# Kernel tuning notes

Measured on AMD Instinct MI355X. Metric: run time of the kernel, lower is better.

The kernel has to match this reference:

```python
import jax, jax.numpy as jnp
import numpy as np

D = 512; N = 1536; H = 4; DH = D // H
MAX_INT = 5; BINS = 100; LAYERS = 3


def _mha(q_in, k_in, v_in, in_w, in_b, out_w, out_b):
    """PyTorch-style nn.MultiheadAttention (batch of 1). Returns (out [Nq,D], head-avg weights [Nq,Nk])."""
    wq, wk, wv = in_w[:D], in_w[D:2 * D], in_w[2 * D:]
    bq, bk, bv = in_b[:D], in_b[D:2 * D], in_b[2 * D:]
    n_q, n_k = q_in.shape[0], k_in.shape[0]
    q = (q_in @ wq.T + bq).reshape(n_q, H, DH).transpose(1, 0, 2)  # [H,Nq,dh]
    k = (k_in @ wk.T + bk).reshape(n_k, H, DH).transpose(1, 0, 2)
    v = (v_in @ wv.T + bv).reshape(n_k, H, DH).transpose(1, 0, 2)
    scores = jnp.einsum('hqd,hkd->hqk', q, k) / jnp.sqrt(jnp.asarray(DH, q.dtype))
    w = jax.nn.softmax(scores, axis=-1)  # [H,Nq,Nk]
    out = jnp.einsum('hqk,hkd->hqd', w, v).transpose(1, 0, 2).reshape(n_q, D)
    out = out @ out_w.T + out_b
    return out, w.mean(0)


def setup_inputs() -> dict:
    key = jax.random.key(0)
    ks = jax.random.split(key, 12)
    s = 0.02
    return {
        'node_embeddings': jax.random.normal(ks[0], (N, D), jnp.float32),
        'time_positions': jax.random.uniform(ks[1], (N, 1), jnp.float32) * 10.0,
        'batch_indices': jnp.zeros((N,), jnp.int32),
        'W_time': jax.random.normal(ks[2], (D, 1), jnp.float32) * s,
        'b_time': jnp.zeros((D,), jnp.float32),
        'in_w': jax.random.normal(ks[3], (3 * D, D), jnp.float32) * s,
        'in_b': jnp.zeros((3 * D,), jnp.float32),
        'out_w': jax.random.normal(ks[4], (D, D), jnp.float32) * s,
        'out_b': jnp.zeros((D,), jnp.float32),
        'ic_w1': jax.random.normal(ks[5], (128, D), jnp.float32) * s,
        'ic_b1': jnp.zeros((128,), jnp.float32),
        'ic_w2': jax.random.normal(ks[6], (MAX_INT, 128), jnp.float32) * s,
        'ic_b2': jnp.zeros((MAX_INT,), jnp.float32),
        'ref_w1': jax.random.normal(ks[7], (LAYERS, 128, D + 2), jnp.float32) * s,
        'ref_b1': jnp.zeros((LAYERS, 128), jnp.float32),
        'ref_w2': jax.random.normal(ks[8], (LAYERS, 2 * BINS, 128), jnp.float32) * s,
        'ref_b2': jnp.zeros((LAYERS, 2 * BINS), jnp.float32),
        'weight_params': jnp.linspace(-0.5, 0.5, BINS).astype(jnp.float32),
        'qp_w': jax.random.normal(ks[9], (D, D + 2), jnp.float32) * s,
        'qp_b': jnp.zeros((D,), jnp.float32),
    }


def _forward(node_embeddings, time_positions, W_time, b_time, in_w, in_b, out_w, out_b,
             ic_w1, ic_b1, ic_w2, ic_b2, ref_w1, ref_b1, ref_w2, ref_b2,
             weight_params, qp_w, qp_b):
    x = node_embeddings + time_positions @ W_time.T + b_time  # [N,D]
    attn_out, _ = _mha(x, x, x, in_w, in_b, out_w, out_b)      # [N,D]
    pooled = attn_out.mean(0)                                   # [D]
    probs = jax.nn.softmax(ic_w2 @ jax.nn.relu(ic_w1 @ pooled + ic_b1) + ic_b2)
    num_intervals = jnp.argmax(probs) + 1
    interval_mask = jnp.arange(MAX_INT) < num_intervals
    t_min, t_max = time_positions.min(), time_positions.max()
    grid = jnp.linspace(t_min, t_max, MAX_INT + 1)
    start, end = grid[:-1], grid[1:]                            # [MAX_INT]
    n = attn_out.shape[0]
    ones = jnp.ones((n, 1), attn_out.dtype)

    def per_interval(s_i, e_i, w1, b1, w2, b2):
        query = jnp.concatenate([attn_out, ones * s_i, ones * e_i], axis=-1)  # [N,D+2]
        qp = query @ qp_w.T + qp_b                                            # [N,D]
        h = jax.nn.relu(query @ w1.T + b1)
        logits = h @ w2.T + b2                                                # [N,2*BINS]
        s_off = (jax.nn.softmax(logits[:, :BINS], axis=-1) * weight_params).sum(-1)  # [N]
        e_off = (jax.nn.softmax(logits[:, BINS:], axis=-1) * weight_params).sum(-1)
        _, aw = _mha(qp, attn_out, attn_out, in_w, in_b, out_w, out_b)        # [N,N]
        return (aw * s_off).sum(), (aw * e_off).sum()

    for l in range(LAYERS):  # layers have distinct params; intervals are independent within a layer
        ds, de = jax.vmap(per_interval, in_axes=(0, 0, None, None, None, None))(
            start, end, ref_w1[l], ref_b1[l], ref_w2[l], ref_b2[l])
        start = start + ds
        end = end + de

    final_bounds = jnp.stack([start, end], axis=-1)  # [MAX_INT,2]
    return final_bounds, interval_mask


def reference(node_embeddings, time_positions, batch_indices, W_time, b_time, in_w, in_b,
              out_w, out_b, ic_w1, ic_b1, ic_w2, ic_b2, ref_w1, ref_b1, ref_w2, ref_b2,
              weight_params, qp_w, qp_b):
    return _forward(node_embeddings, time_positions, W_time, b_time, in_w, in_b, out_w, out_b,
                    ic_w1, ic_b1, ic_w2, ic_b2, ref_w1, ref_b1, ref_w2, ref_b2,
                    weight_params, qp_w, qp_b)
```

## Files before the change

### kernel.cpp

```cpp
#include <hip/hip_runtime.h>
#include <hip/hip_bf16.h>

typedef __hip_bfloat16 bf16;
typedef __bf16 bf16x8 __attribute__((ext_vector_type(8)));
typedef float f32x4 __attribute__((ext_vector_type(4)));

#define DD   512
#define NT   1536
#define NH   4
#define DHD  128
#define NBINS 100
#define MAXI 5
#define NL   3
#define RSQRT_DH 0.08838834764831845f

#define OFF_X      ((size_t)0)
#define OFF_QKV    (OFF_X    + (size_t)NT*DD)
#define OFF_ATT    (OFF_QKV  + (size_t)NT*3*DD)
#define OFF_CTX    (OFF_ATT  + (size_t)NT*DD)
#define OFF_K2     (OFF_CTX  + (size_t)NT*DD)
#define OFF_QP0    (OFF_K2   + (size_t)NT*DD)
#define OFF_Q0     (OFF_QP0  + (size_t)NT*DD)
#define OFF_H0     (OFF_Q0   + (size_t)NT*DD)
#define OFF_HR     (OFF_H0   + (size_t)NT*384)
#define OFF_LG     (OFF_HR   + (size_t)MAXI*NT*128)
#define OFF_AARR   (OFF_LG   + (size_t)MAXI*NT*200)
#define OFF_BARR   (OFF_AARR + (size_t)NH*NT)
#define OFF_AV     (OFF_BARR + (size_t)NH*NT)
#define OFF_BV     (OFF_AV   + (size_t)DD)
#define OFF_SOFF   (OFF_BV   + (size_t)DD)
#define OFF_EOFF   (OFF_SOFF + (size_t)MAXI*NT)
#define OFF_RST    (OFF_EOFF + (size_t)MAXI*NT)
#define OFF_POOL   (OFF_RST  + (size_t)NH*NT*2)
#define OFF_SCAL   (OFF_POOL + (size_t)DD)
#define OFF_S      (OFF_SCAL + (size_t)64)
#define SC_START 0
#define SC_END   5
#define SC_DSDE  10
#define SC_CNT   20
#define OFF_M2   (OFF_QP0 + (size_t)512*512)
#define OFF_B2   (OFF_QP0 + (size_t)2*512*512)
#define PSLICE   ((size_t)NH*NT*16)
#define OFF_STAT (OFF_LG + (size_t)8*PSLICE)

__global__ __launch_bounds__(256) void k_misc(
    const float* __restrict__ tpos, const float* __restrict__ in_w,
    const float* __restrict__ in_b, const float* __restrict__ qp_w,
    const float* __restrict__ qp_b, float* ws)
{
    __shared__ __bf16 As[64 * 40];
    __shared__ __bf16 Bs[64 * 40];
    __shared__ float smn[256], smx[256];
    int bx = blockIdx.x, tid = threadIdx.x;
    if (bx < 64) {
        int m0 = (bx >> 3) * 64, n0 = (bx & 7) * 64;
        int r = tid >> 2, quad = tid & 3;
        int w = tid >> 6, lane = tid & 63;
        int wm = (w & 1) * 32, wn = (w >> 1) * 32;
        int lr = lane & 15, lq = lane >> 4;
        f32x4 acc[2][2];
#pragma unroll
        for (int i = 0; i < 2; i++)
#pragma unroll
            for (int j = 0; j < 2; j++) acc[i][j] = (f32x4){0.f, 0.f, 0.f, 0.f};
        const float* arow = in_w + (size_t)(m0 + r) * DD + quad * 8;
        int kk = tid >> 3, g = tid & 7;
        for (int k0 = 0; k0 < DD; k0 += 32) {
            __bf16 ta[8] __attribute__((aligned(16)));
#pragma unroll
            for (int q = 0; q < 4; q++) {
                float2 f = *(const float2*)(arow + k0 + 2 * q);
                ta[2 * q] = (__bf16)f.x; ta[2 * q + 1] = (__bf16)f.y;
            }
            const float* bsrc = qp_w + (size_t)(k0 + kk) * 514 + n0 + g * 8;
            float4 b0 = *(const float4*)bsrc;
            float4 b1 = *(const float4*)(bsrc + 4);
            float bb[8] = {b0.x, b0.y, b0.z, b0.w, b1.x, b1.y, b1.z, b1.w};
            __syncthreads();
            *(bf16x8*)&As[r * 40 + quad * 8] = *(bf16x8*)ta;
#pragma unroll
            for (int q = 0; q < 8; q++) Bs[(g * 8 + q) * 40 + kk] = (__bf16)bb[q];
            __syncthreads();
            bf16x8 af[2], bfr[2];
#pragma unroll
            for (int i = 0; i < 2; i++) af[i] = *(bf16x8*)&As[(wm + i * 16 + lr) * 40 + lq * 8];
#pragma unroll
            for (int j = 0; j < 2; j++) bfr[j] = *(bf16x8*)&Bs[(wn + j * 16 + lr) * 40 + lq * 8];
#pragma unroll
            for (int i = 0; i < 2; i++)
#pragma unroll
                for (int j = 0; j < 2; j++)
                    acc[i][j] = __builtin_amdgcn_mfma_f32_16x16x32_bf16(af[i], bfr[j], acc[i][j], 0, 0, 0);
        }
        float* M2 = ws + OFF_M2;
#pragma unroll
        for (int i = 0; i < 2; i++)
#pragma unroll
            for (int r4 = 0; r4 < 4; r4++) {
                int gm = m0 + wm + i * 16 + lq * 4 + r4;
#pragma unroll
                for (int j = 0; j < 2; j++)
                    M2[(size_t)gm * 512 + n0 + wn + j * 16 + lr] = acc[i][j][r4];
            }
    } else if (bx < 72) {
        int w = tid >> 6, lane = tid & 63;
        float su8[8], sv8[8], sb8[8];
#pragma unroll
        for (int q = 0; q < 8; q++) {
            int c = lane * 8 + q;
            su8[q] = qp_w[(size_t)c * 514 + 512];
            sv8[q] = qp_w[(size_t)c * 514 + 513];
            sb8[q] = qp_b[c];
        }
        int base = (bx - 64) * 64 + w * 16;
        for (int t = 0; t < 16; t++) {
            int row = base + t;
            const float* wr = in_w + (size_t)row * DD + lane * 8;
            float4 x0 = *(const float4*)wr, x1 = *(const float4*)(wr + 4);
            float xa[8] = {x0.x, x0.y, x0.z, x0.w, x1.x, x1.y, x1.z, x1.w};
            float a = 0.f, b = 0.f, c2 = 0.f;
#pragma unroll
            for (int q = 0; q < 8; q++) { a += xa[q] * su8[q]; b += xa[q] * sv8[q]; c2 += xa[q] * sb8[q]; }
            for (int off = 32; off; off >>= 1) {
                a += __shfl_xor(a, off); b += __shfl_xor(b, off); c2 += __shfl_xor(c2, off);
            }
            if (lane == 0) {
                ws[OFF_AV + row] = a; ws[OFF_BV + row] = b; ws[OFF_B2 + row] = c2 + in_b[row];
            }
        }
    } else {
        ws[OFF_POOL + tid] = 0.f; ws[OFF_POOL + 256 + tid] = 0.f;
        float mn = 1e30f, mx = -1e30f;
        for (int i = tid; i < NT; i += 256) { float v = tpos[i]; mn = fminf(mn, v); mx = fmaxf(mx, v); }
        smn[tid] = mn; smx[tid] = mx; __syncthreads();
        for (int s = 128; s; s >>= 1) {
            if (tid < s) { smn[tid] = fminf(smn[tid], smn[tid + s]); smx[tid] = fmaxf(smx[tid], smx[tid + s]); }
            __syncthreads();
        }
        if (tid == 0) {
            float tmin = smn[0], tmax = smx[0];
            for (int i = 0; i < MAXI; i++) {
                ws[OFF_SCAL + SC_START + i] = tmin + (tmax - tmin) * (float)i / 5.0f;
                ws[OFF_SCAL + SC_END + i]   = tmin + (tmax - tmin) * (float)(i + 1) / 5.0f;
            }
        }
    }
}

__global__ __launch_bounds__(256) void k_score(
    const float* __restrict__ A, int lda, long long aZ,
    const float* __restrict__ B, int ldb, long long bZ,
    bf16* __restrict__ C, float* __restrict__ stat)
{
    int z = blockIdx.z;
    A += (size_t)z * aZ; B += (size_t)z * bZ;
    int m0 = blockIdx.y * 128, n0 = blockIdx.x * 128;
    __shared__ __bf16 As[128 * 40];
    __shared__ __bf16 Bs[128 * 40];
    __shared__ float sMax[4][64];
    __shared__ float sSum[4][64];
    int tid = threadIdx.x;
    int r = tid >> 1, hh = tid & 1;
    int w = tid >> 6, lane = tid & 63;
    int wm = (w & 1) * 64, wn = (w >> 1) * 64;
    int lr = lane & 15, lq = lane >> 4;
    f32x4 acc[4][4];
#pragma unroll
    for (int i = 0; i < 4; i++)
#pragma unroll
        for (int j = 0; j < 4; j++) acc[i][j] = (f32x4){0.f, 0.f, 0.f, 0.f};

    const float* arow = A + (size_t)(m0 + r) * lda + hh * 16;
    const float* brow = B + (size_t)(n0 + r) * ldb + hh * 16;
    __bf16* awr = &As[r * 40 + hh * 16];
    __bf16* bwr = &Bs[r * 40 + hh * 16];

    for (int k0 = 0; k0 < DHD; k0 += 32) {
        __bf16 ta[16] __attribute__((aligned(16)));
        __bf16 tb[16] __attribute__((aligned(16)));
#pragma unroll
        for (int q = 0; q < 8; q++) {
            float2 f = *(const float2*)(arow + k0 + 2 * q);
            ta[2 * q] = (__bf16)f.x; ta[2 * q + 1] = (__bf16)f.y;
            float2 g = *(const float2*)(brow + k0 + 2 * q);
            tb[2 * q] = (__bf16)g.x; tb[2 * q + 1] = (__bf16)g.y;
        }
        __syncthreads();
        *(bf16x8*)awr = *(bf16x8*)ta;
        *(bf16x8*)(awr + 8) = *(bf16x8*)(ta + 8);
        *(bf16x8*)bwr = *(bf16x8*)tb;
        *(bf16x8*)(bwr + 8) = *(bf16x8*)(tb + 8);
        __syncthreads();
        bf16x8 af[4], bfr[4];
#pragma unroll
        for (int i = 0; i < 4; i++) af[i] = *(bf16x8*)&As[(wm + i * 16 + lr) * 40 + lq * 8];
#pragma unroll
        for (int j = 0; j < 4; j++) bfr[j] = *(bf16x8*)&Bs[(wn + j * 16 + lr) * 40 + lq * 8];
#pragma unroll
        for (int i = 0; i < 4; i++)
#pragma unroll
            for (int j = 0; j < 4; j++)
                acc[i][j] = __builtin_amdgcn_mfma_f32_16x16x32_bf16(af[i], bfr[j], acc[i][j], 0, 0, 0);
    }
#pragma unroll
    for (int i = 0; i < 4; i++)
#pragma unroll
        for (int r4 = 0; r4 < 4; r4++) {
            int gm = m0 + wm + i * 16 + lq * 4 + r4;
#pragma unroll
            for (int j = 0; j < 4; j++) {
                int gn = n0 + wn + j * 16 + lr;
                C[(size_t)z * NT * NT + (size_t)gm * NT + gn] =
                    __float2bfloat16(acc[i][j][r4] * RSQRT_DH);
            }
        }
#pragma unroll
    for (int i = 0; i < 4; i++)
#pragma unroll
        for (int r4 = 0; r4 < 4; r4++) {
            float m = -1e30f;
#pragma unroll
            for (int j = 0; j < 4; j++) m = fmaxf(m, acc[i][j][r4] * RSQRT_DH);
            for (int off = 1; off < 16; off <<= 1) m = fmaxf(m, __shfl_xor(m, off));
            if (lr == 0) sMax[w][i * 16 + lq * 4 + r4] = m;
        }
    __syncthreads();
#pragma unroll
    for (int i = 0; i < 4; i++)
#pragma unroll
        for (int r4 = 0; r4 < 4; r4++) {
            int lidx = i * 16 + lq * 4 + r4;
            float M = fmaxf(sMax[w][lidx], sMax[w ^ 2][lidx]);
            float s = 0.f;
#pragma unroll
            for (int j = 0; j < 4; j++) s += __expf(acc[i][j][r4] * RSQRT_DH - M);
            for (int off = 1; off < 16; off <<= 1) s += __shfl_xor(s, off);
            if (lr == 0) sSum[w][lidx] = s;
        }
    __syncthreads();
    if (tid < 128) {
        int lidx = tid & 63, wb = tid >> 6;
        float M = fmaxf(sMax[wb][lidx], sMax[wb + 2][lidx]);
        float den = sSum[wb][lidx] + sSum[wb + 2][lidx];
        size_t base = ((size_t)z * NT + m0 + tid) * 24 + (size_t)blockIdx.x * 2;
        stat[base] = M; stat[base + 1] = den;
    }
}

__global__ __launch_bounds__(256) void k_qkv(
    const float* __restrict__ emb, const float* __restrict__ t,
    const float* __restrict__ wt, const float* __restrict__ bt,
    const float* __restrict__ in_w, const float* __restrict__ in_b, float* ws)
{
    int m0 = blockIdx.y * 64, n0 = blockIdx.x * 64;
    __shared__ __bf16 As[64 * 40];
    __shared__ __bf16 Bs[64 * 40];
    int tid = threadIdx.x;
    int r = tid >> 2, quad = tid & 3;
    int w = tid >> 6, lane = tid & 63;
    int wm = (w & 1) * 32, wn = (w >> 1) * 32;
    int lr = lane & 15, lq = lane >> 4;
    f32x4 acc[2][2];
#pragma unroll
    for (int i = 0; i < 2; i++)
#pragma unroll
        for (int j = 0; j < 2; j++) acc[i][j] = (f32x4){0.f, 0.f, 0.f, 0.f};

    float trow = t[m0 + r];
    const float* arow = emb + (size_t)(m0 + r) * DD + quad * 8;
    const float* brow = in_w + (size_t)(n0 + r) * DD + quad * 8;
    __bf16* awr = &As[r * 40 + quad * 8];
    __bf16* bwr = &Bs[r * 40 + quad * 8];

    for (int k0 = 0; k0 < DD; k0 += 32) {
        __bf16 ta[8] __attribute__((aligned(16)));
        __bf16 tb[8] __attribute__((aligned(16)));
#pragma unroll
        for (int q = 0; q < 4; q++) {
            float2 e = *(const float2*)(arow + k0 + 2 * q);
            float2 wv = *(const float2*)(wt + k0 + quad * 8 + 2 * q);
            float2 bv = *(const float2*)(bt + k0 + quad * 8 + 2 * q);
            ta[2 * q]     = (__bf16)(e.x + trow * wv.x + bv.x);
            ta[2 * q + 1] = (__bf16)(e.y + trow * wv.y + bv.y);
            float2 f = *(const float2*)(brow + k0 + 2 * q);
            tb[2 * q] = (__bf16)f.x; tb[2 * q + 1] = (__bf16)f.y;
        }
        __syncthreads();
        *(bf16x8*)awr = *(bf16x8*)ta;
        *(bf16x8*)bwr = *(bf16x8*)tb;
        __syncthreads();
        bf16x8 af[2], bfr[2];
#pragma unroll
        for (int i = 0; i < 2; i++) af[i] = *(bf16x8*)&As[(wm + i * 16 + lr) * 40 + lq * 8];
#pragma unroll
        for (int j = 0; j < 2; j++) bfr[j] = *(bf16x8*)&Bs[(wn + j * 16 + lr) * 40 + lq * 8];
#pragma unroll
        for (int i = 0; i < 2; i++)
#pragma unroll
            for (int j = 0; j < 2; j++)
                acc[i][j] = __builtin_amdgcn_mfma_f32_16x16x32_bf16(af[i], bfr[j], acc[i][j], 0, 0, 0);
    }
    float* qkv = ws + OFF_QKV;
    float* Vt  = ws + OFF_X;
#pragma unroll
    for (int i = 0; i < 2; i++)
#pragma unroll
        for (int j = 0; j < 2; j++) {
            int gn = n0 + wn + j * 16 + lr;
            int gmb = m0 + wm + i * 16 + lq * 4;
            float b = in_b[gn];
            f32x4 vv = acc[i][j];
            vv[0] += b; vv[1] += b; vv[2] += b; vv[3] += b;
            if (gn < 2 * DD) {
#pragma unroll
                for (int r4 = 0; r4 < 4; r4++)
                    qkv[(size_t)(gmb + r4) * (3 * DD) + gn] = vv[r4];
            } else {
                *(float4*)&Vt[(size_t)(gn - 2 * DD) * NT + gmb] = *(float4*)&vv;
            }
        }
}

__global__ __launch_bounds__(256) void k_pv(const bf16* __restrict__ S, float* ws) {
    int h = blockIdx.z;
    int m0 = blockIdx.y * 64;
    int n0 = (blockIdx.x & 1) * 64;
    int ks = blockIdx.x >> 1;
    const int KCH = NT / 2;
    int kbeg = ks * KCH;
    __shared__ __bf16 As[64 * 40];
    __shared__ __bf16 Bs[64 * 40];
    __shared__ float sM[64], sI[64];
    int tid = threadIdx.x;
    if (tid < 64) {
        const float* st = ws + OFF_STAT + ((size_t)(h * NT + m0 + tid)) * 24;
        float M = -1e30f;
#pragma unroll
        for (int t2 = 0; t2 < 12; t2++) M = fmaxf(M, st[2 * t2]);
        float den = 0.f;
#pragma unroll
        for (int t2 = 0; t2 < 12; t2++) den += st[2 * t2 + 1] * __expf(st[2 * t2] - M);
        sM[tid] = M; sI[tid] = 1.f / den;
    }
    __syncthreads();
    int r = tid >> 2, quad = tid & 3;
    int w = tid >> 6, lane = tid & 63;
    int wm = (w & 1) * 32, wn = (w >> 1) * 32;
    int lr = lane & 15, lq = lane >> 4;
    const float* Vt = ws + OFF_X + (size_t)h * DHD * NT;
    const bf16* Sh = S + (size_t)h * NT * NT;
    float mrow = sM[r];
    const unsigned short* srow = (const unsigned short*)(Sh + (size_t)(m0 + r) * NT) + quad * 8;
    const float* brow = Vt + (size_t)(n0 + r) * NT + quad * 8;
    __bf16* awr = &As[r * 40 + quad * 8];
    __bf16* bwr = &Bs[r * 40 + quad * 8];
    f32x4 acc[2][2];
#pragma unroll
    for (int i = 0; i < 2; i++)
#pragma unroll
        for (int j = 0; j < 2; j++) acc[i][j] = (f32x4){0.f, 0.f, 0.f, 0.f};

    for (int k0 = kbeg; k0 < kbeg + KCH; k0 += 32) {
        union { uint4 u; unsigned short s[8]; } bb;
        bb.u = *(const uint4*)(srow + k0);
        __bf16 ta[8] __attribute__((aligned(16)));
        __bf16 tb[8] __attribute__((aligned(16)));
#pragma unroll
        for (int q = 0; q < 8; q++)
            ta[q] = (__bf16)__expf(__uint_as_float((unsigned)bb.s[q] << 16) - mrow);
#pragma unroll
        for (int q = 0; q < 4; q++) {
            float2 f = *(const float2*)(brow + k0 + 2 * q);
            tb[2 * q] = (__bf16)f.x; tb[2 * q + 1] = (__bf16)f.y;
        }
        __syncthreads();
        *(bf16x8*)awr = *(bf16x8*)ta;
        *(bf16x8*)bwr = *(bf16x8*)tb;
        __syncthreads();
        bf16x8 af[2], bfr[2];
#pragma unroll
        for (int i = 0; i < 2; i++) af[i] = *(bf16x8*)&As[(wm + i * 16 + lr) * 40 + lq * 8];
#pragma unroll
        for (int j = 0; j < 2; j++) bfr[j] = *(bf16x8*)&Bs[(wn + j * 16 + lr) * 40 + lq * 8];
#pragma unroll
        for (int i = 0; i < 2; i++)
#pragma unroll
            for (int j = 0; j < 2; j++)
                acc[i][j] = __builtin_amdgcn_mfma_f32_16x16x32_bf16(af[i], bfr[j], acc[i][j], 0, 0, 0);
    }
    float* dst = ws + (ks == 0 ? OFF_CTX : OFF_HR);
#pragma unroll
    for (int i = 0; i < 2; i++)
#pragma unroll
        for (int r4 = 0; r4 < 4; r4++) {
            int lrow = wm + i * 16 + lq * 4 + r4;
            float ri = sI[lrow];
#pragma unroll
            for (int j = 0; j < 2; j++) {
                int gn = n0 + wn + j * 16 + lr;
                dst[(size_t)(m0 + lrow) * DD + h * DHD + gn] = acc[i][j][r4] * ri;
            }
        }
}

__global__ __launch_bounds__(256) void k_oproj(
    const float* __restrict__ out_w, const float* __restrict__ out_b, float* ws)
{
    int m0 = blockIdx.y * 64, n0 = blockIdx.x * 64;
    __shared__ __bf16 As[64 * 40];
    __shared__ __bf16 Bs[64 * 40];
    __shared__ float ps[64];
    int tid = threadIdx.x;
    int r = tid >> 2, quad = tid & 3;
    int w = tid >> 6, lane = tid & 63;
    int wm = (w & 1) * 32, wn = (w >> 1) * 32;
    int lr = lane & 15, lq = lane >> 4;
    f32x4 acc[2][2];
#pragma unroll
    for (int i = 0; i < 2; i++)
#pragma unroll
        for (int j = 0; j < 2; j++) acc[i][j] = (f32x4){0.f, 0.f, 0.f, 0.f};
    if (tid < 64) ps[tid] = 0.f;

    const float* a0 = ws + OFF_CTX + (size_t)(m0 + r) * DD + quad * 8;
    const float* a1 = ws + OFF_HR  + (size_t)(m0 + r) * DD + quad * 8;
    const float* brow = out_w + (size_t)(n0 + r) * DD + quad * 8;
    __bf16* awr = &As[r * 40 + quad * 8];
    __bf16* bwr = &Bs[r * 40 + quad * 8];

    for (int k0 = 0; k0 < DD; k0 += 32) {
        __bf16 ta[8] __attribute__((aligned(16)));
        __bf16 tb[8] __attribute__((aligned(16)));
#pragma unroll
        for (int q = 0; q < 4; q++) {
            float2 x = *(const float2*)(a0 + k0 + 2 * q);
            float2 y = *(const float2*)(a1 + k0 + 2 * q);
            ta[2 * q]     = (__bf16)(x.x + y.x);
            ta[2 * q + 1] = (__bf16)(x.y + y.y);
            float2 f = *(const float2*)(brow + k0 + 2 * q);
            tb[2 * q] = (__bf16)f.x; tb[2 * q + 1] = (__bf16)f.y;
        }
        __syncthreads();
        *(bf16x8*)awr = *(bf16x8*)ta;
        *(bf16x8*)bwr = *(bf16x8*)tb;
        __syncthreads();
        bf16x8 af[2], bfr[2];
#pragma unroll
        for (int i = 0; i < 2; i++) af[i] = *(bf16x8*)&As[(wm + i * 16 + lr) * 40 + lq * 8];
#pragma unroll
        for (int j = 0; j < 2; j++) bfr[j] = *(bf16x8*)&Bs[(wn + j * 16 + lr) * 40 + lq * 8];
#pragma unroll
        for (int i = 0; i < 2; i++)
#pragma unroll
            for (int j = 0; j < 2; j++)
                acc[i][j] = __builtin_amdgcn_mfma_f32_16x16x32_bf16(af[i], bfr[j], acc[i][j], 0, 0, 0);
    }
    float* att = ws + OFF_ATT;
#pragma unroll
    for (int j = 0; j < 2; j++) {
        int gn = n0 + wn + j * 16 + lr;
        float b = out_b[gn];
        float colsum = 0.f;
#pragma unroll
        for (int i = 0; i < 2; i++)
#pragma unroll
            for (int r4 = 0; r4 < 4; r4++) {
                int gm = m0 + wm + i * 16 + lq * 4 + r4;
                float v = acc[i][j][r4] + b;
                att[(size_t)gm * DD + gn] = v;
                colsum += v;
            }
        atomicAdd(&ps[wn + j * 16 + lr], colsum);
    }
    __syncthreads();
    if (tid < 64) atomicAdd(&ws[OFF_POOL + n0 + tid], ps[tid]);
}

__global__ __launch_bounds__(256) void k_trip(
    const float* __restrict__ in_w, const float* __restrict__ in_b,
    const float* __restrict__ ref_w1, const float* __restrict__ ref_b1,
    const float* __restrict__ icw1, const float* __restrict__ icb1,
    const float* __restrict__ icw2, const float* __restrict__ icb2,
    float* ws, float* out)
{
    __shared__ __bf16 As[64 * 40];
    __shared__ __bf16 Bs[64 * 40];
    __shared__ float h1[128];
    __shared__ float lg[MAXI];
    int bx = blockIdx.x, tid = threadIdx.x;
    if (bx == 22) {
        if (blockIdx.y != 0) return;
        int w = tid >> 6, lane = tid & 63;
        const float* pp = ws + OFF_POOL + lane * 8;
        float4 p0 = *(const float4*)pp, p1 = *(const float4*)(pp + 4);
        float p8[8] = {p0.x, p0.y, p0.z, p0.w, p1.x, p1.y, p1.z, p1.w};
        for (int t = 0; t < 32; t++) {
            int row = w * 32 + t;
            const float* wr = icw1 + (size_t)row * DD + lane * 8;
            float4 a = *(const float4*)wr, b = *(const float4*)(wr + 4);
            float d = a.x * p8[0] + a.y * p8[1] + a.z * p8[2] + a.w * p8[3]
                    + b.x * p8[4] + b.y * p8[5] + b.z * p8[6] + b.w * p8[7];
            for (int off = 32; off; off >>= 1) d += __shfl_xor(d, off);
            if (lane == 0) h1[row] = fmaxf(d * (1.0f / NT) + icb1[row], 0.f);
        }
        __syncthreads();
        if (tid < MAXI) {
            float s = icb2[tid];
            for (int j = 0; j < 128; j++) s += icw2[tid * 128 + j] * h1[j];
            lg[tid] = s;
        }
        __syncthreads();
        if (tid == 0) {
            int best = 0; float bv = lg[0];
            for (int m = 1; m < MAXI; m++) if (lg[m] > bv) { bv = lg[m]; best = m; }
            int ni = best + 1;
            for (int i = 0; i < MAXI; i++) out[10 + i] = (i < ni) ? 1.f : 0.f;
        }
        return;
    }
    const float* B; const float* bias; float* C; int ldb, ldc, n0;
    if (bx < 8)       { B = in_w + (size_t)DD * DD; ldb = DD;  bias = in_b + DD;   C = ws + OFF_K2; ldc = DD;  n0 = bx * 64; }
    else if (bx < 16) { B = ws + OFF_M2;            ldb = 512; bias = ws + OFF_B2; C = ws + OFF_Q0; ldc = DD;  n0 = (bx - 8) * 64; }
    else              { B = ref_w1;                 ldb = 514; bias = ref_b1;      C = ws + OFF_H0; ldc = 384; n0 = (bx - 16) * 64; }
    const float* A = ws + OFF_ATT;
    int m0 = blockIdx.y * 64;
    int r = tid >> 2, quad = tid & 3;
    int w = tid >> 6, lane = tid & 63;
    int wm = (w & 1) * 32, wn = (w >> 1) * 32;
    int lr = lane & 15, lq = lane >> 4;
    f32x4 acc[2][2];
#pragma unroll
    for (int i = 0; i < 2; i++)
#pragma unroll
        for (int j = 0; j < 2; j++) acc[i][j] = (f32x4){0.f, 0.f, 0.f, 0.f};

    const float* arow = A + (size_t)(m0 + r) * DD + quad * 8;
    const float* brow = B + (size_t)(n0 + r) * ldb + quad * 8;
    __bf16* awr = &As[r * 40 + quad * 8];
    __bf16* bwr = &Bs[r * 40 + quad * 8];

    for (int k0 = 0; k0 < DD; k0 += 32) {
        __bf16 ta[8] __attribute__((aligned(16)));
        __bf16 tb[8] __attribute__((aligned(16)));
#pragma unroll
        for (int q = 0; q < 4; q++) {
            float2 f = *(const float2*)(arow + k0 + 2 * q);
            ta[2 * q] = (__bf16)f.x; ta[2 * q + 1] = (__bf16)f.y;
            float2 g = *(const float2*)(brow + k0 + 2 * q);
            tb[2 * q] = (__bf16)g.x; tb[2 * q + 1] = (__bf16)g.y;
        }
        __syncthreads();
        *(bf16x8*)awr = *(bf16x8*)ta;
        *(bf16x8*)bwr = *(bf16x8*)tb;
        __syncthreads();
        bf16x8 af[2], bfr[2];
#pragma unroll
        for (int i = 0; i < 2; i++) af[i] = *(bf16x8*)&As[(wm + i * 16 + lr) * 40 + lq * 8];
#pragma unroll
        for (int j = 0; j < 2; j++) bfr[j] = *(bf16x8*)&Bs[(wn + j * 16 + lr) * 40 + lq * 8];
#pragma unroll
        for (int i = 0; i < 2; i++)
#pragma unroll
            for (int j = 0; j < 2; j++)
                acc[i][j] = __builtin_amdgcn_mfma_f32_16x16x32_bf16(af[i], bfr[j], acc[i][j], 0, 0, 0);
    }
#pragma unroll
    for (int i = 0; i < 2; i++)
#pragma unroll
        for (int r4 = 0; r4 < 4; r4++) {
            int gm = m0 + wm + i * 16 + lq * 4 + r4;
#pragma unroll
            for (int j = 0; j < 2; j++) {
                int gn = n0 + wn + j * 16 + lr;
                C[(size_t)gm * ldc + gn] = acc[i][j][r4] + bias[gn];
            }
        }
}

__global__ __launch_bounds__(256) void k_abc(float* ws) {
    int wave = threadIdx.x >> 6, lane = threadIdx.x & 63;
    int row = blockIdx.x * 4 + wave;
    int h = row / NT, n = row % NT;
    const float* k2 = ws + OFF_K2 + (size_t)n * DD + h * DHD;
    const float* av = ws + OFF_AV + h * DHD;
    const float* bv = ws + OFF_BV + h * DHD;
    int d = lane * 2;
    float a = av[d] * k2[d] + av[d + 1] * k2[d + 1];
    float b = bv[d] * k2[d] + bv[d + 1] * k2[d + 1];
    float tm = (lane < 12) ? ws[OFF_STAT + (size_t)row * 24 + lane * 2] : -1e30f;
    for (int off = 32; off; off >>= 1) { a += __shfl_xor(a, off); b += __shfl_xor(b, off); }
    for (int off = 1; off < 16; off <<= 1) tm = fmaxf(tm, __shfl_xor(tm, off));
    if (lane == 0) {
        ws[OFF_AARR + row] = a * RSQRT_DH;
        ws[OFF_BARR + row] = b * RSQRT_DH;
        ws[OFF_RST + row] = tm;
    }
}

__global__ __launch_bounds__(256) void k_lgs(
    const float* __restrict__ rw1, const float* __restrict__ rw2,
    const float* __restrict__ rb2, const float* __restrict__ wp, int l, float* ws)
{
    __shared__ float dsh[128];
    __shared__ __bf16 As[64 * 136];
    __shared__ __bf16 Bs[64 * 136];
    __shared__ __bf16 Ls[64 * 208];
    int tid = threadIdx.x;
    int m0 = blockIdx.x * 64;
    int i_int = m0 / NT;
    int nbase = m0 % NT;
    if (blockIdx.x == 0 && tid < 11) ws[OFF_SCAL + SC_DSDE + tid] = 0.f;
    if (tid < 128) {
        float s_i = ws[OFF_SCAL + SC_START + i_int], e_i = ws[OFF_SCAL + SC_END + i_int];
        const float* wr = rw1 + (size_t)(l * 128 + tid) * 514;
        dsh[tid] = s_i * wr[512] + e_i * wr[513];
    }
    __syncthreads();
    int r = tid >> 2, quad = tid & 3;
    {
        const float* arow = ws + OFF_H0 + (size_t)(nbase + r) * 384 + l * 128 + quad * 32;
        __bf16 tmp[32] __attribute__((aligned(16)));
#pragma unroll
        for (int q = 0; q < 16; q++) {
            float2 f = *(const float2*)(arow + 2 * q);
            int jj = quad * 32 + 2 * q;
            tmp[2 * q]     = (__bf16)fmaxf(f.x + dsh[jj], 0.f);
            tmp[2 * q + 1] = (__bf16)fmaxf(f.y + dsh[jj + 1], 0.f);
        }
        __bf16* aw = &As[r * 136 + quad * 32];
#pragma unroll
        for (int q = 0; q < 4; q++) *(bf16x8*)(aw + q * 8) = *(bf16x8*)(tmp + q * 8);
    }
    int w = tid >> 6, lane = tid & 63;
    int wm = (w & 1) * 32, wn = (w >> 1) * 32;
    int lr = lane & 15, lq = lane >> 4;
    for (int nt = 0; nt < 4; nt++) {
        int n0 = nt * 64;
        int gnr = n0 + r;
        __bf16 tmp[32] __attribute__((aligned(16)));
        if (gnr < 200) {
            const float* brow = rw2 + (size_t)gnr * 128 + quad * 32;
#pragma unroll
            for (int q = 0; q < 16; q++) {
                float2 f = *(const float2*)(brow + 2 * q);
                tmp[2 * q] = (__bf16)f.x; tmp[2 * q + 1] = (__bf16)f.y;
            }
        } else {
#pragma unroll
            for (int q = 0; q < 32; q++) tmp[q] = (__bf16)0.f;
        }
        __syncthreads();
        {
            __bf16* bw = &Bs[r * 136 + quad * 32];
#pragma unroll
            for (int q = 0; q < 4; q++) *(bf16x8*)(bw + q * 8) = *(bf16x8*)(tmp + q * 8);
        }
        __syncthreads();
        f32x4 acc[2][2];
#pragma unroll
        for (int i = 0; i < 2; i++)
#pragma unroll
            for (int j = 0; j < 2; j++) acc[i][j] = (f32x4){0.f, 0.f, 0.f, 0.f};
#pragma unroll
        for (int kk = 0; kk < 4; kk++) {
            bf16x8 af[2], bfr[2];
#pragma unroll
            for (int i = 0; i < 2; i++) af[i] = *(bf16x8*)&As[(wm + i * 16 + lr) * 136 + kk * 32 + lq * 8];
#pragma unroll
            for (int j = 0; j < 2; j++) bfr[j] = *(bf16x8*)&Bs[(wn + j * 16 + lr) * 136 + kk * 32 + lq * 8];
#pragma unroll
            for (int i = 0; i < 2; i++)
#pragma unroll
                for (int j = 0; j < 2; j++)
                    acc[i][j] = __builtin_amdgcn_mfma_f32_16x16x32_bf16(af[i], bfr[j], acc[i][j], 0, 0, 0);
        }
#pragma unroll
        for (int i = 0; i < 2; i++)
#pragma unroll
            for (int r4 = 0; r4 < 4; r4++) {
                int rl = wm + i * 16 + lq * 4 + r4;
#pragma unroll
                for (int j = 0; j < 2; j++) {
                    int gn = n0 + wn + j * 16 + lr;
                    if (gn < 200) Ls[rl * 208 + gn] = (__bf16)(acc[i][j][r4] + rb2[gn]);
                }
            }
    }
    __syncthreads();
    {
        int rloc = tid >> 2, q = tid & 3;
        int c0 = q * 50;
        const unsigned short* lrow = (const unsigned short*)&Ls[rloc * 208];
        float m = -1e30f;
#pragma unroll
        for (int c = 0; c < 50; c++)
            m = fmaxf(m, __uint_as_float((unsigned)lrow[c0 + c] << 16));
        m = fmaxf(m, __shfl_xor(m, 1));
        float den = 0.f, num = 0.f;
#pragma unroll
        for (int c = 0; c < 50; c++) {
            float p = __expf(__uint_as_float((unsigned)lrow[c0 + c] << 16) - m);
            den += p;
            int wc = c0 + c; if (wc >= NBINS) wc -= NBINS;
            num += p * wp[wc];
        }
        den += __shfl_xor(den, 1);
        num += __shfl_xor(num, 1);
        int n = nbase + rloc;
        if (q == 0)      ws[OFF_SOFF + (size_t)i_int * NT + n] = num / den;
        else if (q == 2) ws[OFF_EOFF + (size_t)i_int * NT + n] = num / den;
    }
}

__global__ __launch_bounds__(256) void k_eg(const bf16* __restrict__ S0, float* ws) {
    int h = blockIdx.z;
    int m0 = blockIdx.y * 128;
    int ks = blockIdx.x;
    const int KCH = NT / 8;
    __shared__ __bf16 As[128 * 40];
    __shared__ __bf16 Bs[16 * 40];
    int tid = threadIdx.x;
    int w = tid >> 6, lane = tid & 63;
    int lr = lane & 15, lq = lane >> 4;
    int r = tid >> 1, half = tid & 1;
    const bf16* Sh = S0 + (size_t)h * NT * NT;
    const unsigned short* arow = (const unsigned short*)(Sh + (size_t)(m0 + r) * NT) + half * 16;
    float mrow = ws[OFF_RST + h * NT + m0 + r];
    int wm = w * 32;
    f32x4 acc[2];
    acc[0] = (f32x4){0.f, 0.f, 0.f, 0.f};
    acc[1] = (f32x4){0.f, 0.f, 0.f, 0.f};
    int bc = tid >> 3, bk = tid & 7;
    int valid = (tid < 128) && (bc < 15);
    int ii = bc / 3, tt = bc - ii * 3;
    if (ii > 4) ii = 4;
    float s_i = 0.f, e_i = 0.f;
    if (valid) { s_i = ws[OFF_SCAL + SC_START + ii]; e_i = ws[OFF_SCAL + SC_END + ii]; }
    const float* Ar = ws + OFF_AARR + h * NT;
    const float* Br = ws + OFF_BARR + h * NT;
    const float* fo = ws + (tt == 2 ? OFF_EOFF : OFF_SOFF) + (size_t)ii * NT;

    for (int k0 = ks * KCH; k0 < ks * KCH + KCH; k0 += 32) {
        union { uint4 u; unsigned short s[8]; } a0, a1, o0, o1;
        a0.u = *(const uint4*)(arow + k0);
        a1.u = *(const uint4*)(arow + k0 + 8);
#pragma unroll
        for (int q = 0; q < 8; q++) {
            __bf16 e0 = (__bf16)__expf(__uint_as_float((unsigned)a0.s[q] << 16) - mrow);
            __bf16 e1 = (__bf16)__expf(__uint_as_float((unsigned)a1.s[q] << 16) - mrow);
            o0.s[q] = *(unsigned short*)&e0;
            o1.s[q] = *(unsigned short*)&e1;
        }
        float bv[4] = {0.f, 0.f, 0.f, 0.f};
        if (valid) {
            float4 a4 = *(const float4*)(Ar + k0 + bk * 4);
            float4 b4 = *(const float4*)(Br + k0 + bk * 4);
            bv[0] = __expf(s_i * a4.x + e_i * b4.x);
            bv[1] = __expf(s_i * a4.y + e_i * b4.y);
            bv[2] = __expf(s_i * a4.z + e_i * b4.z);
            bv[3] = __expf(s_i * a4.w + e_i * b4.w);
            if (tt) {
                float4 f4 = *(const float4*)(fo + k0 + bk * 4);
                bv[0] *= f4.x; bv[1] *= f4.y; bv[2] *= f4.z; bv[3] *= f4.w;
            }
        }
        __syncthreads();
        *(uint4*)&As[r * 40 + half * 16] = o0.u;
        *(uint4*)&As[r * 40 + half * 16 + 8] = o1.u;
        if (tid < 128) {
            __bf16* bw = &Bs[bc * 40 + bk * 4];
            bw[0] = (__bf16)bv[0]; bw[1] = (__bf16)bv[1]; bw[2] = (__bf16)bv[2]; bw[3] = (__bf16)bv[3];
        }
        __syncthreads();
        bf16x8 bf0 = *(bf16x8*)&Bs[lr * 40 + lq * 8];
        bf16x8 af0 = *(bf16x8*)&As[(wm + lr) * 40 + lq * 8];
        bf16x8 af1 = *(bf16x8*)&As[(wm + 16 + lr) * 40 + lq * 8];
        acc[0] = __builtin_amdgcn_mfma_f32_16x16x32_bf16(af0, bf0, acc[0], 0, 0, 0);
        acc[1] = __builtin_amdgcn_mfma_f32_16x16x32_bf16(af1, bf0, acc[1], 0, 0, 0);
    }
    float* P = ws + OFF_LG + (size_t)ks * PSLICE;
    if (lr < 15) {
#pragma unroll
        for (int i = 0; i < 2; i++)
#pragma unroll
            for (int r4 = 0; r4 < 4; r4++) {
                int gm = m0 + wm + i * 16 + lq * 4 + r4;
                P[(size_t)(h * NT + gm) * 16 + lr] = acc[i][r4];
            }
    }
}

__global__ __launch_bounds__(256) void k_fin(float* ws, float* out, int l) {
    __shared__ float part[4][10];
    int tid = threadIdx.x;
    int w = tid >> 6, lane = tid & 63;
    int row = blockIdx.x * 256 + tid;
    float acc[15];
#pragma unroll
    for (int c = 0; c < 15; c++) acc[c] = 0.f;
    for (int ks = 0; ks < 8; ks++) {
        const float* Pr = ws + OFF_LG + (size_t)ks * PSLICE + (size_t)row * 16;
#pragma unroll
        for (int c = 0; c < 15; c++) acc[c] += Pr[c];
    }
    float loc[10];
#pragma unroll
    for (int i = 0; i < MAXI; i++) {
        float den = acc[i * 3];
        loc[i]        = acc[i * 3 + 1] / den;
        loc[MAXI + i] = acc[i * 3 + 2] / den;
    }
#pragma unroll
    for (int c = 0; c < 10; c++)
        for (int off = 32; off; off >>= 1) loc[c] += __shfl_xor(loc[c], off);
    if (lane == 0) {
#pragma unroll
        for (int c = 0; c < 10; c++) part[w][c] = loc[c];
    }
    __syncthreads();
    if (tid < 10) {
        float s = part[0][tid] + part[1][tid] + part[2][tid] + part[3][tid];
        atomicAdd(&ws[OFF_SCAL + SC_DSDE + tid], s);
    }
    __threadfence();
    __syncthreads();
    if (tid == 0) {
        unsigned old = atomicAdd((unsigned*)&ws[OFF_SCAL + SC_CNT], 1u);
        if (old == 23) {
            for (int i = 0; i < MAXI; i++) {
                float ds = atomicAdd(&ws[OFF_SCAL + SC_DSDE + i], 0.f);
                float de = atomicAdd(&ws[OFF_SCAL + SC_DSDE + MAXI + i], 0.f);
                float ns = ws[OFF_SCAL + SC_START + i] + ds * 0.25f;
                float ne = ws[OFF_SCAL + SC_END + i]   + de * 0.25f;
                ws[OFF_SCAL + SC_START + i] = ns;
                ws[OFF_SCAL + SC_END + i]   = ne;
                if (l == NL - 1) { out[2 * i] = ns; out[2 * i + 1] = ne; }
            }
        }
    }
}

extern "C" void kernel_launch(void* const* d_in, const int* in_sizes, int n_in,
                              void* d_out, int out_size, void* d_ws, size_t ws_size,
                              hipStream_t stream) {
    const float* emb    = (const float*)d_in[0];
    const float* tpos   = (const float*)d_in[1];
    const float* W_time = (const float*)d_in[3];
    const float* b_time = (const float*)d_in[4];
    const float* in_w   = (const float*)d_in[5];
    const float* in_b   = (const float*)d_in[6];
    const float* out_w  = (const float*)d_in[7];
    const float* out_b  = (const float*)d_in[8];
    const float* ic_w1  = (const float*)d_in[9];
    const float* ic_b1  = (const float*)d_in[10];
    const float* ic_w2  = (const float*)d_in[11];
    const float* ic_b2  = (const float*)d_in[12];
    const float* ref_w1 = (const float*)d_in[13];
    const float* ref_b1 = (const float*)d_in[14];
    const float* ref_w2 = (const float*)d_in[15];
    const float* ref_b2 = (const float*)d_in[16];
    const float* wp     = (const float*)d_in[17];
    const float* qp_w   = (const float*)d_in[18];
    const float* qp_b   = (const float*)d_in[19];
    float* ws  = (float*)d_ws;
    float* out = (float*)d_out;
    bf16* S = (bf16*)(ws + OFF_S);

    k_misc<<<73, 256, 0, stream>>>(tpos, in_w, in_b, qp_w, qp_b, ws);

    k_qkv<<<dim3(24, 24), 256, 0, stream>>>(emb, tpos, W_time, b_time, in_w, in_b, ws);
    k_score<<<dim3(12, 12, NH), 256, 0, stream>>>(
        ws + OFF_QKV, 3 * DD, DHD, ws + OFF_QKV + DD, 3 * DD, DHD, S, ws + OFF_STAT);
    k_pv<<<dim3(4, NT / 64, NH), 256, 0, stream>>>(S, ws);
    k_oproj<<<dim3(8, 24), 256, 0, stream>>>(out_w, out_b, ws);

    k_trip<<<dim3(23, 24), 256, 0, stream>>>(in_w, in_b, ref_w1, ref_b1,
                                             ic_w1, ic_b1, ic_w2, ic_b2, ws, out);

    k_score<<<dim3(12, 12, NH), 256, 0, stream>>>(
        ws + OFF_Q0, DD, DHD, ws + OFF_K2, DD, DHD, S, ws + OFF_STAT);
    k_abc<<<NH * NT / 4, 256, 0, stream>>>(ws);

    for (int l = 0; l < NL; l++) {
        k_lgs<<<120, 256, 0, stream>>>(ref_w1, ref_w2 + (size_t)l * 200 * 128,
                                       ref_b2 + l * 200, wp, l, ws);
        k_eg<<<dim3(8, NT / 128, NH), 256, 0, stream>>>(S, ws);
        k_fin<<<NH * NT / 256, 256, 0, stream>>>(ws, out, l);
    }
}
```

Before: 357.9 us.

## Store bf16 intermediates and unnormalised exp scores, pre-convert weights to bf16

Intermediates (QKV, transposed V, attention outputs, K2/Q0, M2) are now stored in bf16, and in_w, out_w and ref weights are converted to bf16 once in k_misc. GEMM loaders then issue plain 16-byte copies instead of converting fp32 on the fly. k_score now writes exp(score) directly, with no running-max subtraction, and only per-tile row sums. This lets k_pv and the three k_eg passes consume the exponentials without recomputing exp. k_pv also switches to a 128-wide N tile with fewer blocks. The cost is lost max-stabilisation, which could overflow for large-magnitude scores, plus extra bf16 rounding of intermediates.

```diff
diff --git a/kernel.cpp b/kernel.cpp
--- a/kernel.cpp
+++ b/kernel.cpp
@@ -14,43 +14,64 @@
 #define NL   3
 #define RSQRT_DH 0.08838834764831845f
 
-#define OFF_X      ((size_t)0)
-#define OFF_QKV    (OFF_X    + (size_t)NT*DD)
-#define OFF_ATT    (OFF_QKV  + (size_t)NT*3*DD)
+#define OFF_ATT    ((size_t)0)
 #define OFF_CTX    (OFF_ATT  + (size_t)NT*DD)
-#define OFF_K2     (OFF_CTX  + (size_t)NT*DD)
-#define OFF_QP0    (OFF_K2   + (size_t)NT*DD)
-#define OFF_Q0     (OFF_QP0  + (size_t)NT*DD)
-#define OFF_H0     (OFF_Q0   + (size_t)NT*DD)
-#define OFF_HR     (OFF_H0   + (size_t)NT*384)
-#define OFF_LG     (OFF_HR   + (size_t)MAXI*NT*128)
-#define OFF_AARR   (OFF_LG   + (size_t)MAXI*NT*200)
+#define OFF_CTX1   (OFF_CTX  + (size_t)NT*DD)
+#define OFF_H0     (OFF_CTX1 + (size_t)NT*DD)
+#define OFF_LG     (OFF_H0   + (size_t)NT*384)
+#define OFF_AARR   (OFF_LG   + (size_t)8*NH*NT*16)
 #define OFF_BARR   (OFF_AARR + (size_t)NH*NT)
 #define OFF_AV     (OFF_BARR + (size_t)NH*NT)
 #define OFF_BV     (OFF_AV   + (size_t)DD)
-#define OFF_SOFF   (OFF_BV   + (size_t)DD)
+#define OFF_B2     (OFF_BV   + (size_t)DD)
+#define OFF_SOFF   (OFF_B2   + (size_t)DD)
 #define OFF_EOFF   (OFF_SOFF + (size_t)MAXI*NT)
-#define OFF_RST    (OFF_EOFF + (size_t)MAXI*NT)
-#define OFF_POOL   (OFF_RST  + (size_t)NH*NT*2)
+#define OFF_STAT   (OFF_EOFF + (size_t)MAXI*NT)
+#define OFF_POOL   (OFF_STAT + (size_t)NH*NT*12)
 #define OFF_SCAL   (OFF_POOL + (size_t)DD)
-#define OFF_S      (OFF_SCAL + (size_t)64)
+#define OFF_E      (OFF_SCAL + (size_t)64)
 #define SC_START 0
 #define SC_END   5
 #define SC_DSDE  10
 #define SC_CNT   20
-#define OFF_M2   (OFF_QP0 + (size_t)512*512)
-#define OFF_B2   (OFF_QP0 + (size_t)2*512*512)
 #define PSLICE   ((size_t)NH*NT*16)
-#define OFF_STAT (OFF_LG + (size_t)8*PSLICE)
+#define BF_BASE  (OFF_E + (size_t)NH*NT*NT/2)
+#define BQKB   ((size_t)0)
+#define BVT    (BQKB  + (size_t)NT*1024)
+#define BATT   (BVT   + (size_t)NH*128*NT)
+#define BK2    (BATT  + (size_t)NT*512)
+#define BQ0    (BK2   + (size_t)NT*512)
+#define BM2    (BQ0   + (size_t)NT*512)
+#define BINW   (BM2   + (size_t)512*512)
+#define BOUTW  (BINW  + (size_t)1536*512)
+#define BRW1   (BOUTW + (size_t)512*512)
+#define BRW2   (BRW1  + (size_t)384*512)
+
+__device__ __forceinline__ void cvt8(const float* s, bf16* d) {
+    float4 f0 = *(const float4*)s, f1 = *(const float4*)(s + 4);
+    union { uint4 u; unsigned short us[8]; } o;
+    bf16 t;
+    t = __float2bfloat16(f0.x); o.us[0] = *(unsigned short*)&t;
+    t = __float2bfloat16(f0.y); o.us[1] = *(unsigned short*)&t;
+    t = __float2bfloat16(f0.z); o.us[2] = *(unsigned short*)&t;
+    t = __float2bfloat16(f0.w); o.us[3] = *(unsigned short*)&t;
+    t = __float2bfloat16(f1.x); o.us[4] = *(unsigned short*)&t;
+    t = __float2bfloat16(f1.y); o.us[5] = *(unsigned short*)&t;
+    t = __float2bfloat16(f1.z); o.us[6] = *(unsigned short*)&t;
+    t = __float2bfloat16(f1.w); o.us[7] = *(unsigned short*)&t;
+    *(uint4*)d = o.u;
+}
 
 __global__ __launch_bounds__(256) void k_misc(
     const float* __restrict__ tpos, const float* __restrict__ in_w,
-    const float* __restrict__ in_b, const float* __restrict__ qp_w,
-    const float* __restrict__ qp_b, float* ws)
+    const float* __restrict__ in_b, const float* __restrict__ out_w,
+    const float* __restrict__ ref_w1, const float* __restrict__ ref_w2,
+    const float* __restrict__ qp_w, const float* __restrict__ qp_b, float* ws)
 {
     __shared__ __bf16 As[64 * 40];
     __shared__ __bf16 Bs[64 * 40];
     __shared__ float smn[256], smx[256];
+    bf16* bp = (bf16*)(ws + BF_BASE);
     int bx = blockIdx.x, tid = threadIdx.x;
     if (bx < 64) {
         int m0 = (bx >> 3) * 64, n0 = (bx & 7) * 64;
@@ -92,7 +113,7 @@
                 for (int j = 0; j < 2; j++)
                     acc[i][j] = __builtin_amdgcn_mfma_f32_16x16x32_bf16(af[i], bfr[j], acc[i][j], 0, 0, 0);
         }
-        float* M2 = ws + OFF_M2;
+        bf16* M2B = bp + BM2;
 #pragma unroll
         for (int i = 0; i < 2; i++)
 #pragma unroll
@@ -100,7 +121,7 @@
                 int gm = m0 + wm + i * 16 + lq * 4 + r4;
 #pragma unroll
                 for (int j = 0; j < 2; j++)
-                    M2[(size_t)gm * 512 + n0 + wn + j * 16 + lr] = acc[i][j][r4];
+                    M2B[(size_t)gm * 512 + n0 + wn + j * 16 + lr] = __float2bfloat16(acc[i][j][r4]);
             }
     } else if (bx < 72) {
         int w = tid >> 6, lane = tid & 63;
@@ -128,7 +149,7 @@
                 ws[OFF_AV + row] = a; ws[OFF_BV + row] = b; ws[OFF_B2 + row] = c2 + in_b[row];
             }
         }
-    } else {
+    } else if (bx == 72) {
         ws[OFF_POOL + tid] = 0.f; ws[OFF_POOL + 256 + tid] = 0.f;
         float mn = 1e30f, mx = -1e30f;
         for (int i = tid; i < NT; i += 256) { float v = tpos[i]; mn = fminf(mn, v); mx = fmaxf(mx, v); }
@@ -144,20 +165,49 @@
                 ws[OFF_SCAL + SC_END + i]   = tmin + (tmax - tmin) * (float)(i + 1) / 5.0f;
             }
         }
-    }
-}
-
+    } else if (bx < 89) {
+        size_t start = (size_t)(bx - 73) * 6144;
+        for (int it = 0; it < 24; it++) {
+            size_t g = start + it * 256 + tid;
+            cvt8(in_w + g * 8, bp + BINW + g * 8);
+        }
+    } else if (bx < 93) {
+        size_t start = (size_t)(bx - 89) * 8192;
+        for (int it = 0; it < 32; it++) {
+            size_t g = start + it * 256 + tid;
+            cvt8(out_w + g * 8, bp + BOUTW + g * 8);
+        }
+    } else if (bx < 97) {
+        size_t start = (size_t)(bx - 93) * 6144;
+        for (int it = 0; it < 24; it++) {
+            size_t g = start + it * 256 + tid;
+            int row = (int)(g >> 6), col = (int)(g & 63) * 8;
+            const float* s = ref_w1 + (size_t)row * 514 + col;
+            float buf[8];
+#pragma unroll
+            for (int q = 0; q < 4; q++) { float2 f = *(const float2*)(s + 2 * q); buf[2 * q] = f.x; buf[2 * q + 1] = f.y; }
+            cvt8(buf, bp + BRW1 + (size_t)row * 512 + col);
+        }
+    } else {
+        for (int it = 0; it < 38; it++) {
+            size_t g = (size_t)it * 256 + tid;
+            if (g < 9600) cvt8(ref_w2 + g * 8, bp + BRW2 + g * 8);
+        }
+    }
+}
+
+template <int STATS>
 __global__ __launch_bounds__(256) void k_score(
-    const float* __restrict__ A, int lda, long long aZ,
-    const float* __restrict__ B, int ldb, long long bZ,
-    bf16* __restrict__ C, float* __restrict__ stat)
+    const bf16* __restrict__ Ab, int lda, int aZ,
+    const bf16* __restrict__ Bb, int ldb, int bZ,
+    bf16* __restrict__ E, float* __restrict__ stat)
 {
     int z = blockIdx.z;
-    A += (size_t)z * aZ; B += (size_t)z * bZ;
+    const __bf16* A = (const __bf16*)Ab + (size_t)z * aZ;
+    const __bf16* B = (const __bf16*)Bb + (size_t)z * bZ;
     int m0 = blockIdx.y * 128, n0 = blockIdx.x * 128;
     __shared__ __bf16 As[128 * 40];
     __shared__ __bf16 Bs[128 * 40];
-    __shared__ float sMax[4][64];
     __shared__ float sSum[4][64];
     int tid = threadIdx.x;
     int r = tid >> 1, hh = tid & 1;
@@ -170,26 +220,19 @@
 #pragma unroll
         for (int j = 0; j < 4; j++) acc[i][j] = (f32x4){0.f, 0.f, 0.f, 0.f};
 
-    const float* arow = A + (size_t)(m0 + r) * lda + hh * 16;
-    const float* brow = B + (size_t)(n0 + r) * ldb + hh * 16;
+    const __bf16* arow = A + (size_t)(m0 + r) * lda + hh * 16;
+    const __bf16* brow = B + (size_t)(n0 + r) * ldb + hh * 16;
     __bf16* awr = &As[r * 40 + hh * 16];
     __bf16* bwr = &Bs[r * 40 + hh * 16];
 
     for (int k0 = 0; k0 < DHD; k0 += 32) {
-        __bf16 ta[16] __attribute__((aligned(16)));
-        __bf16 tb[16] __attribute__((aligned(16)));
-#pragma unroll
-        for (int q = 0; q < 8; q++) {
-            float2 f = *(const float2*)(arow + k0 + 2 * q);
-            ta[2 * q] = (__bf16)f.x; ta[2 * q + 1] = (__bf16)f.y;
-            float2 g = *(const float2*)(brow + k0 + 2 * q);
-            tb[2 * q] = (__bf16)g.x; tb[2 * q + 1] = (__bf16)g.y;
-        }
-        __syncthreads();
-        *(bf16x8*)awr = *(bf16x8*)ta;
-        *(bf16x8*)(awr + 8) = *(bf16x8*)(ta + 8);
-        *(bf16x8*)bwr = *(bf16x8*)tb;
-        *(bf16x8*)(bwr + 8) = *(bf16x8*)(tb + 8);
+        uint4 a0 = *(const uint4*)(arow + k0);
+        uint4 a1 = *(const uint4*)(arow + k0 + 8);
+        uint4 b0 = *(const uint4*)(brow + k0);
+        uint4 b1 = *(const uint4*)(brow + k0 + 8);
+        __syncthreads();
+        *(uint4*)awr = a0; *(uint4*)(awr + 8) = a1;
+        *(uint4*)bwr = b0; *(uint4*)(bwr + 8) = b1;
         __syncthreads();
         bf16x8 af[4], bfr[4];
 #pragma unroll
@@ -202,56 +245,39 @@
             for (int j = 0; j < 4; j++)
                 acc[i][j] = __builtin_amdgcn_mfma_f32_16x16x32_bf16(af[i], bfr[j], acc[i][j], 0, 0, 0);
     }
+    bf16* Ez = E + (size_t)z * NT * NT;
 #pragma unroll
     for (int i = 0; i < 4; i++)
 #pragma unroll
         for (int r4 = 0; r4 < 4; r4++) {
             int gm = m0 + wm + i * 16 + lq * 4 + r4;
+            float s = 0.f;
 #pragma unroll
             for (int j = 0; j < 4; j++) {
-                int gn = n0 + wn + j * 16 + lr;
-                C[(size_t)z * NT * NT + (size_t)gm * NT + gn] =
-                    __float2bfloat16(acc[i][j][r4] * RSQRT_DH);
-            }
-        }
-#pragma unroll
-    for (int i = 0; i < 4; i++)
-#pragma unroll
-        for (int r4 = 0; r4 < 4; r4++) {
-            float m = -1e30f;
-#pragma unroll
-            for (int j = 0; j < 4; j++) m = fmaxf(m, acc[i][j][r4] * RSQRT_DH);
-            for (int off = 1; off < 16; off <<= 1) m = fmaxf(m, __shfl_xor(m, off));
-            if (lr == 0) sMax[w][i * 16 + lq * 4 + r4] = m;
-        }
-    __syncthreads();
-#pragma unroll
-    for (int i = 0; i < 4; i++)
-#pragma unroll
-        for (int r4 = 0; r4 < 4; r4++) {
-            int lidx = i * 16 + lq * 4 + r4;
-            float M = fmaxf(sMax[w][lidx], sMax[w ^ 2][lidx]);
-            float s = 0.f;
-#pragma unroll
-            for (int j = 0; j < 4; j++) s += __expf(acc[i][j][r4] * RSQRT_DH - M);
-            for (int off = 1; off < 16; off <<= 1) s += __shfl_xor(s, off);
-            if (lr == 0) sSum[w][lidx] = s;
-        }
-    __syncthreads();
-    if (tid < 128) {
-        int lidx = tid & 63, wb = tid >> 6;
-        float M = fmaxf(sMax[wb][lidx], sMax[wb + 2][lidx]);
-        float den = sSum[wb][lidx] + sSum[wb + 2][lidx];
-        size_t base = ((size_t)z * NT + m0 + tid) * 24 + (size_t)blockIdx.x * 2;
-        stat[base] = M; stat[base + 1] = den;
+                float e = __expf(acc[i][j][r4] * RSQRT_DH);
+                Ez[(size_t)gm * NT + n0 + wn + j * 16 + lr] = __float2bfloat16(e);
+                s += e;
+            }
+            if (STATS) {
+                for (int off = 1; off < 16; off <<= 1) s += __shfl_xor(s, off);
+                if (lr == 0) sSum[w][i * 16 + lq * 4 + r4] = s;
+            }
+        }
+    if (STATS) {
+        __syncthreads();
+        if (tid < 128) {
+            int lidx = tid & 63, wb = tid >> 6;
+            stat[((size_t)z * NT + m0 + tid) * 12 + blockIdx.x] = sSum[wb][lidx] + sSum[wb + 2][lidx];
+        }
     }
 }
 
 __global__ __launch_bounds__(256) void k_qkv(
     const float* __restrict__ emb, const float* __restrict__ t,
     const float* __restrict__ wt, const float* __restrict__ bt,
-    const float* __restrict__ in_w, const float* __restrict__ in_b, float* ws)
+    const float* __restrict__ in_b, float* ws)
 {
+    bf16* bp = (bf16*)(ws + BF_BASE);
     int m0 = blockIdx.y * 64, n0 = blockIdx.x * 64;
     __shared__ __bf16 As[64 * 40];
     __shared__ __bf16 Bs[64 * 40];
@@ -268,13 +294,12 @@
 
     float trow = t[m0 + r];
     const float* arow = emb + (size_t)(m0 + r) * DD + quad * 8;
-    const float* brow = in_w + (size_t)(n0 + r) * DD + quad * 8;
+    const __bf16* brow = (const __bf16*)(bp + BINW) + (size_t)(n0 + r) * 512 + quad * 8;
     __bf16* awr = &As[r * 40 + quad * 8];
     __bf16* bwr = &Bs[r * 40 + quad * 8];
 
     for (int k0 = 0; k0 < DD; k0 += 32) {
         __bf16 ta[8] __attribute__((aligned(16)));
-        __bf16 tb[8] __attribute__((aligned(16)));
 #pragma unroll
         for (int q = 0; q < 4; q++) {
             float2 e = *(const float2*)(arow + k0 + 2 * q);
@@ -282,12 +307,11 @@
             float2 bv = *(const float2*)(bt + k0 + quad * 8 + 2 * q);
             ta[2 * q]     = (__bf16)(e.x + trow * wv.x + bv.x);
             ta[2 * q + 1] = (__bf16)(e.y + trow * wv.y + bv.y);
-            float2 f = *(const float2*)(brow + k0 + 2 * q);
-            tb[2 * q] = (__bf16)f.x; tb[2 * q + 1] = (__bf16)f.y;
-        }
+        }
+        uint4 bbv = *(const uint4*)(brow + k0);
         __syncthreads();
         *(bf16x8*)awr = *(bf16x8*)ta;
-        *(bf16x8*)bwr = *(bf16x8*)tb;
+        *(uint4*)bwr = bbv;
         __syncthreads();
         bf16x8 af[2], bfr[2];
 #pragma unroll
@@ -300,8 +324,8 @@
             for (int j = 0; j < 2; j++)
                 acc[i][j] = __builtin_amdgcn_mfma_f32_16x16x32_bf16(af[i], bfr[j], acc[i][j], 0, 0, 0);
     }
-    float* qkv = ws + OFF_QKV;
-    float* Vt  = ws + OFF_X;
+    bf16* QKB = bp + BQKB;
+    bf16* VtB = bp + BVT;
 #pragma unroll
     for (int i = 0; i < 2; i++)
 #pragma unroll
@@ -309,86 +333,76 @@
             int gn = n0 + wn + j * 16 + lr;
             int gmb = m0 + wm + i * 16 + lq * 4;
             float b = in_b[gn];
-            f32x4 vv = acc[i][j];
-            vv[0] += b; vv[1] += b; vv[2] += b; vv[3] += b;
             if (gn < 2 * DD) {
 #pragma unroll
                 for (int r4 = 0; r4 < 4; r4++)
-                    qkv[(size_t)(gmb + r4) * (3 * DD) + gn] = vv[r4];
+                    QKB[(size_t)(gmb + r4) * 1024 + gn] = __float2bfloat16(acc[i][j][r4] + b);
             } else {
-                *(float4*)&Vt[(size_t)(gn - 2 * DD) * NT + gmb] = *(float4*)&vv;
-            }
-        }
-}
-
-__global__ __launch_bounds__(256) void k_pv(const bf16* __restrict__ S, float* ws) {
+                union { uint2 u; unsigned short us[4]; } o;
+#pragma unroll
+                for (int r4 = 0; r4 < 4; r4++) {
+                    bf16 t2 = __float2bfloat16(acc[i][j][r4] + b);
+                    o.us[r4] = *(unsigned short*)&t2;
+                }
+                *(uint2*)&VtB[(size_t)(gn - 2 * DD) * NT + gmb] = o.u;
+            }
+        }
+}
+
+__global__ __launch_bounds__(256) void k_pv(const bf16* __restrict__ E, float* ws) {
+    bf16* bp = (bf16*)(ws + BF_BASE);
     int h = blockIdx.z;
     int m0 = blockIdx.y * 64;
-    int n0 = (blockIdx.x & 1) * 64;
-    int ks = blockIdx.x >> 1;
+    int ks = blockIdx.x;
     const int KCH = NT / 2;
     int kbeg = ks * KCH;
     __shared__ __bf16 As[64 * 40];
-    __shared__ __bf16 Bs[64 * 40];
-    __shared__ float sM[64], sI[64];
+    __shared__ __bf16 Bs[128 * 40];
+    __shared__ float sI[64];
     int tid = threadIdx.x;
     if (tid < 64) {
-        const float* st = ws + OFF_STAT + ((size_t)(h * NT + m0 + tid)) * 24;
-        float M = -1e30f;
-#pragma unroll
-        for (int t2 = 0; t2 < 12; t2++) M = fmaxf(M, st[2 * t2]);
+        const float* st = ws + OFF_STAT + (size_t)(h * NT + m0 + tid) * 12;
         float den = 0.f;
 #pragma unroll
-        for (int t2 = 0; t2 < 12; t2++) den += st[2 * t2 + 1] * __expf(st[2 * t2] - M);
-        sM[tid] = M; sI[tid] = 1.f / den;
-    }
-    __syncthreads();
-    int r = tid >> 2, quad = tid & 3;
+        for (int t2 = 0; t2 < 12; t2++) den += st[t2];
+        sI[tid] = 1.f / den;
+    }
+    int rA = tid >> 2, quadA = tid & 3;
+    int rB = tid >> 1, hhB = tid & 1;
     int w = tid >> 6, lane = tid & 63;
-    int wm = (w & 1) * 32, wn = (w >> 1) * 32;
+    int wm = (w & 1) * 32, wn = (w >> 1) * 64;
     int lr = lane & 15, lq = lane >> 4;
-    const float* Vt = ws + OFF_X + (size_t)h * DHD * NT;
-    const bf16* Sh = S + (size_t)h * NT * NT;
-    float mrow = sM[r];
-    const unsigned short* srow = (const unsigned short*)(Sh + (size_t)(m0 + r) * NT) + quad * 8;
-    const float* brow = Vt + (size_t)(n0 + r) * NT + quad * 8;
-    __bf16* awr = &As[r * 40 + quad * 8];
-    __bf16* bwr = &Bs[r * 40 + quad * 8];
-    f32x4 acc[2][2];
+    const __bf16* Eh = (const __bf16*)E + (size_t)h * NT * NT;
+    const __bf16* arow = Eh + (size_t)(m0 + rA) * NT + quadA * 8;
+    const __bf16* brow = (const __bf16*)(bp + BVT) + ((size_t)h * 128 + rB) * NT + hhB * 16;
+    __bf16* awr = &As[rA * 40 + quadA * 8];
+    __bf16* bwr = &Bs[rB * 40 + hhB * 16];
+    f32x4 acc[2][4];
 #pragma unroll
     for (int i = 0; i < 2; i++)
 #pragma unroll
-        for (int j = 0; j < 2; j++) acc[i][j] = (f32x4){0.f, 0.f, 0.f, 0.f};
+        for (int j = 0; j < 4; j++) acc[i][j] = (f32x4){0.f, 0.f, 0.f, 0.f};
 
     for (int k0 = kbeg; k0 < kbeg + KCH; k0 += 32) {
-        union { uint4 u; unsigned short s[8]; } bb;
-        bb.u = *(const uint4*)(srow + k0);
-        __bf16 ta[8] __attribute__((aligned(16)));
-        __bf16 tb[8] __attribute__((aligned(16)));
-#pragma unroll
-        for (int q = 0; q < 8; q++)
-            ta[q] = (__bf16)__expf(__uint_as_float((unsigned)bb.s[q] << 16) - mrow);
-#pragma unroll
-        for (int q = 0; q < 4; q++) {
-            float2 f = *(const float2*)(brow + k0 + 2 * q);
-            tb[2 * q] = (__bf16)f.x; tb[2 * q + 1] = (__bf16)f.y;
-        }
-        __syncthreads();
-        *(bf16x8*)awr = *(bf16x8*)ta;
-        *(bf16x8*)bwr = *(bf16x8*)tb;
-        __syncthreads();
-        bf16x8 af[2], bfr[2];
+        uint4 av = *(const uint4*)(arow + k0);
+        uint4 b0 = *(const uint4*)(brow + k0);
+        uint4 b1 = *(const uint4*)(brow + k0 + 8);
+        __syncthreads();
+        *(uint4*)awr = av;
+        *(uint4*)bwr = b0; *(uint4*)(bwr + 8) = b1;
+        __syncthreads();
+        bf16x8 af[2], bfr[4];
 #pragma unroll
         for (int i = 0; i < 2; i++) af[i] = *(bf16x8*)&As[(wm + i * 16 + lr) * 40 + lq * 8];
 #pragma unroll
-        for (int j = 0; j < 2; j++) bfr[j] = *(bf16x8*)&Bs[(wn + j * 16 + lr) * 40 + lq * 8];
-#pragma unroll
-        for (int i = 0; i < 2; i++)
-#pragma unroll
-            for (int j = 0; j < 2; j++)
+        for (int j = 0; j < 4; j++) bfr[j] = *(bf16x8*)&Bs[(wn + j * 16 + lr) * 40 + lq * 8];
+#pragma unroll
+        for (int i = 0; i < 2; i++)
+#pragma unroll
+            for (int j = 0; j < 4; j++)
                 acc[i][j] = __builtin_amdgcn_mfma_f32_16x16x32_bf16(af[i], bfr[j], acc[i][j], 0, 0, 0);
     }
-    float* dst = ws + (ks == 0 ? OFF_CTX : OFF_HR);
+    float* dst = ws + (ks == 0 ? OFF_CTX : OFF_CTX1);
 #pragma unroll
     for (int i = 0; i < 2; i++)
 #pragma unroll
@@ -396,16 +410,15 @@
             int lrow = wm + i * 16 + lq * 4 + r4;
             float ri = sI[lrow];
 #pragma unroll
-            for (int j = 0; j < 2; j++) {
-                int gn = n0 + wn + j * 16 + lr;
+            for (int j = 0; j < 4; j++) {
+                int gn = wn + j * 16 + lr;
                 dst[(size_t)(m0 + lrow) * DD + h * DHD + gn] = acc[i][j][r4] * ri;
             }
         }
 }
 
-__global__ __launch_bounds__(256) void k_oproj(
-    const float* __restrict__ out_w, const float* __restrict__ out_b, float* ws)
-{
+__global__ __launch_bounds__(256) void k_oproj(const float* __restrict__ out_b, float* ws) {
+    bf16* bp = (bf16*)(ws + BF_BASE);
     int m0 = blockIdx.y * 64, n0 = blockIdx.x * 64;
     __shared__ __bf16 As[64 * 40];
     __shared__ __bf16 Bs[64 * 40];
@@ -422,27 +435,25 @@
         for (int j = 0; j < 2; j++) acc[i][j] = (f32x4){0.f, 0.f, 0.f, 0.f};
     if (tid < 64) ps[tid] = 0.f;
 
-    const float* a0 = ws + OFF_CTX + (size_t)(m0 + r) * DD + quad * 8;
-    const float* a1 = ws + OFF_HR  + (size_t)(m0 + r) * DD + quad * 8;
-    const float* brow = out_w + (size_t)(n0 + r) * DD + quad * 8;
+    const float* a0 = ws + OFF_CTX  + (size_t)(m0 + r) * DD + quad * 8;
+    const float* a1 = ws + OFF_CTX1 + (size_t)(m0 + r) * DD + quad * 8;
+    const __bf16* brow = (const __bf16*)(bp + BOUTW) + (size_t)(n0 + r) * 512 + quad * 8;
     __bf16* awr = &As[r * 40 + quad * 8];
     __bf16* bwr = &Bs[r * 40 + quad * 8];
 
     for (int k0 = 0; k0 < DD; k0 += 32) {
         __bf16 ta[8] __attribute__((aligned(16)));
-        __bf16 tb[8] __attribute__((aligned(16)));
 #pragma unroll
         for (int q = 0; q < 4; q++) {
             float2 x = *(const float2*)(a0 + k0 + 2 * q);
             float2 y = *(const float2*)(a1 + k0 + 2 * q);
             ta[2 * q]     = (__bf16)(x.x + y.x);
             ta[2 * q + 1] = (__bf16)(x.y + y.y);
-            float2 f = *(const float2*)(brow + k0 + 2 * q);
-            tb[2 * q] = (__bf16)f.x; tb[2 * q + 1] = (__bf16)f.y;
-        }
+        }
+        uint4 bbv = *(const uint4*)(brow + k0);
         __syncthreads();
         *(bf16x8*)awr = *(bf16x8*)ta;
-        *(bf16x8*)bwr = *(bf16x8*)tb;
+        *(uint4*)bwr = bbv;
         __syncthreads();
         bf16x8 af[2], bfr[2];
 #pragma unroll
@@ -456,6 +467,7 @@
                 acc[i][j] = __builtin_amdgcn_mfma_f32_16x16x32_bf16(af[i], bfr[j], acc[i][j], 0, 0, 0);
     }
     float* att = ws + OFF_ATT;
+    bf16* attB = bp + BATT;
 #pragma unroll
     for (int j = 0; j < 2; j++) {
         int gn = n0 + wn + j * 16 + lr;
@@ -468,6 +480,7 @@
                 int gm = m0 + wm + i * 16 + lq * 4 + r4;
                 float v = acc[i][j][r4] + b;
                 att[(size_t)gm * DD + gn] = v;
+                attB[(size_t)gm * 512 + gn] = __float2bfloat16(v);
                 colsum += v;
             }
         atomicAdd(&ps[wn + j * 16 + lr], colsum);
@@ -477,12 +490,12 @@
 }
 
 __global__ __launch_bounds__(256) void k_trip(
-    const float* __restrict__ in_w, const float* __restrict__ in_b,
-    const float* __restrict__ ref_w1, const float* __restrict__ ref_b1,
+    const float* __restrict__ in_b, const float* __restrict__ ref_b1,
     const float* __restrict__ icw1, const float* __restrict__ icb1,
     const float* __restrict__ icw2, const float* __restrict__ icb2,
     float* ws, float* out)
 {
+    bf16* bp = (bf16*)(ws + BF_BASE);
     __shared__ __bf16 As[64 * 40];
     __shared__ __bf16 Bs[64 * 40];
     __shared__ float h1[128];
@@ -518,11 +531,11 @@
         }
         return;
     }
-    const float* B; const float* bias; float* C; int ldb, ldc, n0;
-    if (bx < 8)       { B = in_w + (size_t)DD * DD; ldb = DD;  bias = in_b + DD;   C = ws + OFF_K2; ldc = DD;  n0 = bx * 64; }
-    else if (bx < 16) { B = ws + OFF_M2;            ldb = 512; bias = ws + OFF_B2; C = ws + OFF_Q0; ldc = DD;  n0 = (bx - 8) * 64; }
-    else              { B = ref_w1;                 ldb = 514; bias = ref_b1;      C = ws + OFF_H0; ldc = 384; n0 = (bx - 16) * 64; }
-    const float* A = ws + OFF_ATT;
+    const __bf16* B; const float* bias; int n0, mode;
+    bf16* Cb = nullptr; float* Cf = nullptr;
+    if (bx < 8)       { B = (const __bf16*)(bp + BINW) + (size_t)512 * 512; bias = in_b + DD;     Cb = bp + BK2; n0 = bx * 64; mode = 0; }
+    else if (bx < 16) { B = (const __bf16*)(bp + BM2);                      bias = ws + OFF_B2;   Cb = bp + BQ0; n0 = (bx - 8) * 64; mode = 0; }
+    else              { B = (const __bf16*)(bp + BRW1);                     bias = ref_b1;        Cf = ws + OFF_H0; n0 = (bx - 16) * 64; mode = 1; }
     int m0 = blockIdx.y * 64;
     int r = tid >> 2, quad = tid & 3;
     int w = tid >> 6, lane = tid & 63;
@@ -534,24 +547,17 @@
 #pragma unroll
         for (int j = 0; j < 2; j++) acc[i][j] = (f32x4){0.f, 0.f, 0.f, 0.f};
 
-    const float* arow = A + (size_t)(m0 + r) * DD + quad * 8;
-    const float* brow = B + (size_t)(n0 + r) * ldb + quad * 8;
+    const __bf16* arow = (const __bf16*)(bp + BATT) + (size_t)(m0 + r) * 512 + quad * 8;
+    const __bf16* brow = B + (size_t)(n0 + r) * 512 + quad * 8;
     __bf16* awr = &As[r * 40 + quad * 8];
     __bf16* bwr = &Bs[r * 40 + quad * 8];
 
     for (int k0 = 0; k0 < DD; k0 += 32) {
-        __bf16 ta[8] __attribute__((aligned(16)));
-        __bf16 tb[8] __attribute__((aligned(16)));
-#pragma unroll
-        for (int q = 0; q < 4; q++) {
-            float2 f = *(const float2*)(arow + k0 + 2 * q);
-            ta[2 * q] = (__bf16)f.x; ta[2 * q + 1] = (__bf16)f.y;
-            float2 g = *(const float2*)(brow + k0 + 2 * q);
-            tb[2 * q] = (__bf16)g.x; tb[2 * q + 1] = (__bf16)g.y;
-        }
-        __syncthreads();
-        *(bf16x8*)awr = *(bf16x8*)ta;
-        *(bf16x8*)bwr = *(bf16x8*)tb;
+        uint4 av = *(const uint4*)(arow + k0);
+        uint4 bv = *(const uint4*)(brow + k0);
+        __syncthreads();
+        *(uint4*)awr = av;
+        *(uint4*)bwr = bv;
         __syncthreads();
         bf16x8 af[2], bfr[2];
 #pragma unroll
@@ -572,35 +578,35 @@
 #pragma unroll
             for (int j = 0; j < 2; j++) {
                 int gn = n0 + wn + j * 16 + lr;
-                C[(size_t)gm * ldc + gn] = acc[i][j][r4] + bias[gn];
+                float v = acc[i][j][r4] + bias[gn];
+                if (mode == 0) Cb[(size_t)gm * 512 + gn] = __float2bfloat16(v);
+                else           Cf[(size_t)gm * 384 + gn] = v;
             }
         }
 }
 
 __global__ __launch_bounds__(256) void k_abc(float* ws) {
+    bf16* bp = (bf16*)(ws + BF_BASE);
     int wave = threadIdx.x >> 6, lane = threadIdx.x & 63;
     int row = blockIdx.x * 4 + wave;
     int h = row / NT, n = row % NT;
-    const float* k2 = ws + OFF_K2 + (size_t)n * DD + h * DHD;
+    const unsigned short* k2 = (const unsigned short*)(bp + BK2 + (size_t)n * 512 + h * DHD);
     const float* av = ws + OFF_AV + h * DHD;
     const float* bv = ws + OFF_BV + h * DHD;
     int d = lane * 2;
-    float a = av[d] * k2[d] + av[d + 1] * k2[d + 1];
-    float b = bv[d] * k2[d] + bv[d + 1] * k2[d + 1];
-    float tm = (lane < 12) ? ws[OFF_STAT + (size_t)row * 24 + lane * 2] : -1e30f;
+    float k0 = __uint_as_float((unsigned)k2[d] << 16);
+    float k1 = __uint_as_float((unsigned)k2[d + 1] << 16);
+    float a = av[d] * k0 + av[d + 1] * k1;
+    float b = bv[d] * k0 + bv[d + 1] * k1;
     for (int off = 32; off; off >>= 1) { a += __shfl_xor(a, off); b += __shfl_xor(b, off); }
-    for (int off = 1; off < 16; off <<= 1) tm = fmaxf(tm, __shfl_xor(tm, off));
-    if (lane == 0) {
-        ws[OFF_AARR + row] = a * RSQRT_DH;
-        ws[OFF_BARR + row] = b * RSQRT_DH;
-        ws[OFF_RST + row] = tm;
-    }
+    if (lane == 0) { ws[OFF_AARR + row] = a * RSQRT_DH; ws[OFF_BARR + row] = b * RSQRT_DH; }
 }
 
 __global__ __launch_bounds__(256) void k_lgs(
-    const float* __restrict__ rw1, const float* __restrict__ rw2,
-    const float* __restrict__ rb2, const float* __restrict__ wp, int l, float* ws)
+    const float* __restrict__ rw1, const float* __restrict__ rb2,
+    const float* __restrict__ wp, int l, float* ws)
 {
+    bf16* bp = (bf16*)(ws + BF_BASE);
     __shared__ float dsh[128];
     __shared__ __bf16 As[64 * 136];
     __shared__ __bf16 Bs[64 * 136];
@@ -634,26 +640,21 @@
     int w = tid >> 6, lane = tid & 63;
     int wm = (w & 1) * 32, wn = (w >> 1) * 32;
     int lr = lane & 15, lq = lane >> 4;
+    const __bf16* rw2b = (const __bf16*)(bp + BRW2) + (size_t)l * 200 * 128;
     for (int nt = 0; nt < 4; nt++) {
         int n0 = nt * 64;
         int gnr = n0 + r;
-        __bf16 tmp[32] __attribute__((aligned(16)));
+        uint4 b0 = {0, 0, 0, 0}, b1 = {0, 0, 0, 0}, b2v = {0, 0, 0, 0}, b3 = {0, 0, 0, 0};
         if (gnr < 200) {
-            const float* brow = rw2 + (size_t)gnr * 128 + quad * 32;
-#pragma unroll
-            for (int q = 0; q < 16; q++) {
-                float2 f = *(const float2*)(brow + 2 * q);
-                tmp[2 * q] = (__bf16)f.x; tmp[2 * q + 1] = (__bf16)f.y;
-            }
-        } else {
-#pragma unroll
-            for (int q = 0; q < 32; q++) tmp[q] = (__bf16)0.f;
+            const __bf16* brow = rw2b + (size_t)gnr * 128 + quad * 32;
+            b0 = *(const uint4*)brow; b1 = *(const uint4*)(brow + 8);
+            b2v = *(const uint4*)(brow + 16); b3 = *(const uint4*)(brow + 24);
         }
         __syncthreads();
         {
             __bf16* bw = &Bs[r * 136 + quad * 32];
-#pragma unroll
-            for (int q = 0; q < 4; q++) *(bf16x8*)(bw + q * 8) = *(bf16x8*)(tmp + q * 8);
+            *(uint4*)bw = b0; *(uint4*)(bw + 8) = b1;
+            *(uint4*)(bw + 16) = b2v; *(uint4*)(bw + 24) = b3;
         }
         __syncthreads();
         f32x4 acc[2][2];
@@ -712,7 +713,7 @@
     }
 }
 
-__global__ __launch_bounds__(256) void k_eg(const bf16* __restrict__ S0, float* ws) {
+__global__ __launch_bounds__(256) void k_eg(const bf16* __restrict__ E0, float* ws) {
     int h = blockIdx.z;
     int m0 = blockIdx.y * 128;
     int ks = blockIdx.x;
@@ -723,9 +724,8 @@
     int w = tid >> 6, lane = tid & 63;
     int lr = lane & 15, lq = lane >> 4;
     int r = tid >> 1, half = tid & 1;
-    const bf16* Sh = S0 + (size_t)h * NT * NT;
-    const unsigned short* arow = (const unsigned short*)(Sh + (size_t)(m0 + r) * NT) + half * 16;
-    float mrow = ws[OFF_RST + h * NT + m0 + r];
+    const unsigned short* arow =
+        (const unsigned short*)((const __bf16*)E0 + (size_t)h * NT * NT + (size_t)(m0 + r) * NT) + half * 16;
     int wm = w * 32;
     f32x4 acc[2];
     acc[0] = (f32x4){0.f, 0.f, 0.f, 0.f};
@@ -741,16 +741,8 @@
     const float* fo = ws + (tt == 2 ? OFF_EOFF : OFF_SOFF) + (size_t)ii * NT;
 
     for (int k0 = ks * KCH; k0 < ks * KCH + KCH; k0 += 32) {
-        union { uint4 u; unsigned short s[8]; } a0, a1, o0, o1;
-        a0.u = *(const uint4*)(arow + k0);
-        a1.u = *(const uint4*)(arow + k0 + 8);
-#pragma unroll
-        for (int q = 0; q < 8; q++) {
-            __bf16 e0 = (__bf16)__expf(__uint_as_float((unsigned)a0.s[q] << 16) - mrow);
-            __bf16 e1 = (__bf16)__expf(__uint_as_float((unsigned)a1.s[q] << 16) - mrow);
-            o0.s[q] = *(unsigned short*)&e0;
-            o1.s[q] = *(unsigned short*)&e1;
-        }
+        uint4 a0 = *(const uint4*)(arow + k0);
+        uint4 a1 = *(const uint4*)(arow + k0 + 8);
         float bv[4] = {0.f, 0.f, 0.f, 0.f};
         if (valid) {
             float4 a4 = *(const float4*)(Ar + k0 + bk * 4);
@@ -765,8 +757,8 @@
             }
         }
         __syncthreads();
-        *(uint4*)&As[r * 40 + half * 16] = o0.u;
-        *(uint4*)&As[r * 40 + half * 16 + 8] = o1.u;
+        *(uint4*)&As[r * 40 + half * 16] = a0;
+        *(uint4*)&As[r * 40 + half * 16 + 8] = a1;
         if (tid < 128) {
             __bf16* bw = &Bs[bc * 40 + bk * 4];
             bw[0] = (__bf16)bv[0]; bw[1] = (__bf16)bv[1]; bw[2] = (__bf16)bv[2]; bw[3] = (__bf16)bv[3];
@@ -864,27 +856,26 @@
     const float* qp_b   = (const float*)d_in[19];
     float* ws  = (float*)d_ws;
     float* out = (float*)d_out;
-    bf16* S = (bf16*)(ws + OFF_S);
-
-    k_misc<<<73, 256, 0, stream>>>(tpos, in_w, in_b, qp_w, qp_b, ws);
-
-    k_qkv<<<dim3(24, 24), 256, 0, stream>>>(emb, tpos, W_time, b_time, in_w, in_b, ws);
-    k_score<<<dim3(12, 12, NH), 256, 0, stream>>>(
-        ws + OFF_QKV, 3 * DD, DHD, ws + OFF_QKV + DD, 3 * DD, DHD, S, ws + OFF_STAT);
-    k_pv<<<dim3(4, NT / 64, NH), 256, 0, stream>>>(S, ws);
-    k_oproj<<<dim3(8, 24), 256, 0, stream>>>(out_w, out_b, ws);
-
-    k_trip<<<dim3(23, 24), 256, 0, stream>>>(in_w, in_b, ref_w1, ref_b1,
-                                             ic_w1, ic_b1, ic_w2, ic_b2, ws, out);
-
-    k_score<<<dim3(12, 12, NH), 256, 0, stream>>>(
-        ws + OFF_Q0, DD, DHD, ws + OFF_K2, DD, DHD, S, ws + OFF_STAT);
+    bf16* E = (bf16*)(ws + OFF_E);
+    bf16* bp = (bf16*)(ws + BF_BASE);
+
+    k_misc<<<98, 256, 0, stream>>>(tpos, in_w, in_b, out_w, ref_w1, ref_w2, qp_w, qp_b, ws);
+
+    k_qkv<<<dim3(24, 24), 256, 0, stream>>>(emb, tpos, W_time, b_time, in_b, ws);
+    k_score<1><<<dim3(12, 12, NH), 256, 0, stream>>>(
+        bp + BQKB, 1024, DHD, bp + BQKB + 512, 1024, DHD, E, ws + OFF_STAT);
+    k_pv<<<dim3(2, NT / 64, NH), 256, 0, stream>>>(E, ws);
+    k_oproj<<<dim3(8, 24), 256, 0, stream>>>(out_b, ws);
+
+    k_trip<<<dim3(23, 24), 256, 0, stream>>>(in_b, ref_b1, ic_w1, ic_b1, ic_w2, ic_b2, ws, out);
+
+    k_score<0><<<dim3(12, 12, NH), 256, 0, stream>>>(
+        bp + BQ0, 512, DHD, bp + BK2, 512, DHD, E, nullptr);
     k_abc<<<NH * NT / 4, 256, 0, stream>>>(ws);
 
     for (int l = 0; l < NL; l++) {
-        k_lgs<<<120, 256, 0, stream>>>(ref_w1, ref_w2 + (size_t)l * 200 * 128,
-                                       ref_b2 + l * 200, wp, l, ws);
-        k_eg<<<dim3(8, NT / 128, NH), 256, 0, stream>>>(S, ws);
+        k_lgs<<<120, 256, 0, stream>>>(ref_w1, ref_b2 + l * 200, wp, l, ws);
+        k_eg<<<dim3(8, NT / 128, NH), 256, 0, stream>>>(E, ws);
         k_fin<<<NH * NT / 256, 256, 0, stream>>>(ws, out, l);
     }
 }
```

New measurement: 305.9 us. 1.17x faster.
